# Optimization experiments

Hardware: AMD Instinct MI355X
Metric: run time of the kernel (lower is better)

## Reference

```python
import jax, jax.numpy as jnp
import numpy as np

D_MODEL = 512
N_HEADS = 8
D_K = D_MODEL // N_HEADS


def setup_inputs() -> dict:
    key = jax.random.key(0)
    ks = jax.random.split(key, 9)
    s = 1.0 / np.sqrt(D_MODEL)
    x = jax.random.normal(ks[0], (2, 4096, D_MODEL), dtype=jnp.float32)
    def lin(kw, kb):
        W = jax.random.uniform(kw, (D_MODEL, D_MODEL), jnp.float32, -s, s)
        b = jax.random.uniform(kb, (D_MODEL,), jnp.float32, -s, s)
        return W, b
    Wq, bq = lin(ks[1], ks[2])
    Wk, bk = lin(ks[3], ks[4])
    Wv, bv = lin(ks[5], ks[6])
    Wo, bo = lin(ks[7], ks[8])
    return {"x": x, "Wq": Wq, "bq": bq, "Wk": Wk, "bk": bk,
            "Wv": Wv, "bv": bv, "Wo": Wo, "bo": bo}


def reference(x, Wq, bq, Wk, bk, Wv, bv, Wo, bo):
    B, T, C = x.shape
    # project and split heads: [B, H, T, d_k]
    def heads(W, b):
        return (x @ W.T + b).reshape(B, T, N_HEADS, D_K).transpose(0, 2, 1, 3)
    q = heads(Wq, bq)
    k = heads(Wk, bk)
    v = heads(Wv, bv)
    scores = jnp.einsum('bhqd,bhkd->bhqk', q, k) / np.sqrt(D_K).astype(jnp.float32)
    attn = jax.nn.softmax(scores, axis=-1)  # dropout p=0 (eval)
    out = jnp.einsum('bhqk,bhkd->bhqd', attn, v)
    out = out.transpose(0, 2, 1, 3).reshape(B, T, C)
    return out @ Wo.T + bo
```

## Files before the change

kernel.cpp:

```cpp
#include <hip/hip_runtime.h>

typedef _Float16 f16x8 __attribute__((ext_vector_type(8)));
typedef _Float16 f16x4 __attribute__((ext_vector_type(4)));
typedef _Float16 f16x2 __attribute__((ext_vector_type(2)));
typedef __fp16 hf16x2 __attribute__((ext_vector_type(2)));
typedef float f32x4 __attribute__((ext_vector_type(4)));

__device__ __forceinline__ float fast_exp2(float x) {
#if __has_builtin(__builtin_amdgcn_exp2f)
  return __builtin_amdgcn_exp2f(x);
#else
  return exp2f(x);
#endif
}

__device__ __forceinline__ f16x2 pk_cvt(float a, float b) {
#if __has_builtin(__builtin_amdgcn_cvt_pkrtz)
  union { hf16x2 h; f16x2 f; } u;
  u.h = __builtin_amdgcn_cvt_pkrtz(a, b);
  return u.f;
#else
  f16x2 r; r[0] = (_Float16)a; r[1] = (_Float16)b; return r;
#endif
}

__global__ void cvt_all(const float* __restrict__ x,
                        const float* __restrict__ Wq, const float* __restrict__ Wk,
                        const float* __restrict__ Wv, const float* __restrict__ Wo,
                        _Float16* __restrict__ xf, _Float16* __restrict__ wf) {
  int g = blockIdx.x * blockDim.x + threadIdx.x;
  const float* src;
  _Float16* dst;
  if (g < 524288) {
    src = x + (size_t)g * 8;
    dst = xf + (size_t)g * 8;
  } else {
    int g2 = g - 524288;
    int z = g2 >> 15, off = g2 & 32767;
    const float* W = (z == 0) ? Wq : (z == 1) ? Wk : (z == 2) ? Wv : Wo;
    src = W + (size_t)off * 8;
    dst = wf + (size_t)z * 262144 + (size_t)off * 8;
  }
  f32x4 a = *(const f32x4*)src;
  f32x4 b = *(const f32x4*)(src + 4);
  f16x8 o;
  o[0] = (_Float16)a[0]; o[1] = (_Float16)a[1];
  o[2] = (_Float16)a[2]; o[3] = (_Float16)a[3];
  o[4] = (_Float16)b[0]; o[5] = (_Float16)b[1];
  o[6] = (_Float16)b[2]; o[7] = (_Float16)b[3];
  *(f16x8*)dst = o;
}

__global__ __launch_bounds__(256, 2)
void qkv_gemm(const _Float16* __restrict__ X, const _Float16* __restrict__ Wf,
              const float* __restrict__ bq, const float* __restrict__ bk,
              const float* __restrict__ bv, _Float16* __restrict__ dst3) {
  __shared__ __align__(16) _Float16 As[128][72];
  __shared__ __align__(16) _Float16 Bs[128][72];
  const int z = blockIdx.z;
  const _Float16* Wz = Wf + (size_t)z * 262144;
  const float* bias = (z == 0) ? bq : (z == 1 ? bk : bv);
  _Float16* dst = dst3 + (size_t)z * 4194304;
  const float scale = (z == 0) ? 0.18033688011112042f : 1.0f;

  const int t = threadIdx.x;
  const int lane = t & 63, wave = t >> 6;
  const int quad = lane >> 4, col = lane & 15;
  const int wm = (wave & 1) * 64, wn = (wave >> 1) * 64;
  const int m0 = blockIdx.x * 128, n0 = blockIdx.y * 128;

  f32x4 acc[4][4] = {};

  for (int k0 = 0; k0 < 512; k0 += 64) {
    __syncthreads();
#pragma unroll
    for (int i = 0; i < 4; i++) {
      int flat = i * 2048 + t * 8;
      int r = flat >> 6, c = flat & 63;
      *(f16x8*)&As[r][c] = *(const f16x8*)&X[(size_t)(m0 + r) * 512 + k0 + c];
      *(f16x8*)&Bs[r][c] = *(const f16x8*)&Wz[(size_t)(n0 + r) * 512 + k0 + c];
    }
    __syncthreads();
#pragma unroll
    for (int ks = 0; ks < 2; ks++) {
      f16x8 a[4], b[4];
#pragma unroll
      for (int i = 0; i < 4; i++) {
        a[i] = *(const f16x8*)&As[wm + i * 16 + col][ks * 32 + quad * 8];
        b[i] = *(const f16x8*)&Bs[wn + i * 16 + col][ks * 32 + quad * 8];
      }
#pragma unroll
      for (int mi = 0; mi < 4; mi++)
#pragma unroll
        for (int ni = 0; ni < 4; ni++)
          acc[mi][ni] = __builtin_amdgcn_mfma_f32_16x16x32_f16(a[mi], b[ni], acc[mi][ni], 0, 0, 0);
    }
  }

  if (z != 2) {
#pragma unroll
    for (int ni = 0; ni < 4; ni++) {
      int n = n0 + wn + ni * 16 + col;
      float bv_ = bias[n];
      int h = n >> 6, d = n & 63;
#pragma unroll
      for (int mi = 0; mi < 4; mi++) {
#pragma unroll
        for (int r = 0; r < 4; r++) {
          int m = m0 + wm + mi * 16 + quad * 4 + r;
          int b = m >> 12, tt = m & 4095;
          float v = (acc[mi][ni][r] + bv_) * scale;
          dst[((size_t)(b * 8 + h) * 4096 + tt) * 64 + d] = (_Float16)v;
        }
      }
    }
  } else {
#pragma unroll
    for (int ni = 0; ni < 4; ni++) {
      int n = n0 + wn + ni * 16 + col;
      float bv_ = bias[n];
      int h = n >> 6, d = n & 63;
#pragma unroll
      for (int mi = 0; mi < 4; mi++) {
        int m = m0 + wm + mi * 16 + quad * 4;
        int b = m >> 12, tt = m & 4095;
        f16x4 ov;
#pragma unroll
        for (int r = 0; r < 4; r++) ov[r] = (_Float16)(acc[mi][ni][r] + bv_);
        *(f16x4*)&dst[((size_t)((b * 8 + h) * 64 + d)) * 4096 + tt] = ov;
      }
    }
  }
}

__global__ __launch_bounds__(256, 2)
void attn_kernel(const _Float16* __restrict__ Q, const _Float16* __restrict__ K,
                 const _Float16* __restrict__ V, _Float16* __restrict__ O) {
  __shared__ __align__(16) _Float16 Ks[2][128][72];
  __shared__ __align__(16) _Float16 Vt[2][64][132];

  const int t = threadIdx.x;
  const int lane = t & 63, wave = t >> 6;
  const int quad = lane >> 4, col = lane & 15;
  const int bh = blockIdx.y;
  const int q0 = blockIdx.x * 128;
  const _Float16* Qb = Q + (size_t)bh * 4096 * 64;
  const _Float16* Kbh = K + (size_t)bh * 4096 * 64;
  const _Float16* Vg = V + (size_t)bh * 64 * 4096;

  const int sr = (t * 8) >> 6, sc = (t * 8) & 63;
  const int vrow = t >> 4, vcol = (t & 15) * 8;

  f16x8 qf[2][2];
#pragma unroll
  for (int mt = 0; mt < 2; mt++)
#pragma unroll
    for (int ks = 0; ks < 2; ks++)
      qf[mt][ks] = *(const f16x8*)&Qb[(size_t)(q0 + wave * 32 + mt * 16 + col) * 64 +
                                      ks * 32 + quad * 8];

  const f32x4 fz = {0.f, 0.f, 0.f, 0.f};

  f16x8 kreg[4], vreg[4];
#pragma unroll
  for (int i = 0; i < 4; i++)
    kreg[i] = *(const f16x8*)&Kbh[(size_t)(sr + 32 * i) * 64 + sc];
#pragma unroll
  for (int it = 0; it < 4; it++)
    vreg[it] = *(const f16x8*)&Vg[(size_t)(it * 16 + vrow) * 4096 + vcol];
#pragma unroll
  for (int i = 0; i < 4; i++)
    *(f16x8*)&Ks[0][sr + 32 * i][sc] = kreg[i];
#pragma unroll
  for (int it = 0; it < 4; it++) {
    f16x4 lo, hi;
#pragma unroll
    for (int u = 0; u < 4; u++) { lo[u] = vreg[it][u]; hi[u] = vreg[it][u + 4]; }
    *(f16x4*)&Vt[0][it * 16 + vrow][vcol] = lo;
    *(f16x4*)&Vt[0][it * 16 + vrow][vcol + 4] = hi;
  }
  __syncthreads();

  f32x4 o_acc[2][4] = {};
  float lsum[2] = {0.f, 0.f};

  for (int j = 0; j < 32; j++) {
    const int buf = j & 1;
    if (j + 1 < 32) {
      const _Float16* Kb = Kbh + (size_t)(j + 1) * 128 * 64;
#pragma unroll
      for (int i = 0; i < 4; i++)
        kreg[i] = *(const f16x8*)&Kb[(size_t)(sr + 32 * i) * 64 + sc];
#pragma unroll
      for (int it = 0; it < 4; it++)
        vreg[it] = *(const f16x8*)&Vg[(size_t)(it * 16 + vrow) * 4096 +
                                      (j + 1) * 128 + vcol];
    }

    f32x4 s[2][8];
    __builtin_amdgcn_s_setprio(1);
#pragma unroll
    for (int nt = 0; nt < 8; nt++) {
      f16x8 kf = *(const f16x8*)&Ks[buf][nt * 16 + col][quad * 8];
#pragma unroll
      for (int mt = 0; mt < 2; mt++)
        s[mt][nt] = __builtin_amdgcn_mfma_f32_16x16x32_f16(kf, qf[mt][0], fz, 0, 0, 0);
    }
#pragma unroll
    for (int nt = 0; nt < 8; nt++) {
      f16x8 kf = *(const f16x8*)&Ks[buf][nt * 16 + col][32 + quad * 8];
#pragma unroll
      for (int mt = 0; mt < 2; mt++)
        s[mt][nt] = __builtin_amdgcn_mfma_f32_16x16x32_f16(kf, qf[mt][1], s[mt][nt], 0, 0, 0);
    }
    __builtin_amdgcn_s_setprio(0);

    f16x4 pf[2][8];
#pragma unroll
    for (int mt = 0; mt < 2; mt++) {
#pragma unroll
      for (int nt = 0; nt < 8; nt++) {
        float p0 = fast_exp2(s[mt][nt][0]);
        float p1 = fast_exp2(s[mt][nt][1]);
        float p2 = fast_exp2(s[mt][nt][2]);
        float p3 = fast_exp2(s[mt][nt][3]);
        lsum[mt] += (p0 + p1) + (p2 + p3);
        union { f16x4 v4; f16x2 v2[2]; } u;
        u.v2[0] = pk_cvt(p0, p1);
        u.v2[1] = pk_cvt(p2, p3);
        pf[mt][nt] = u.v4;
      }
    }

    __builtin_amdgcn_s_setprio(1);
#pragma unroll
    for (int nt = 0; nt < 8; nt++) {
#pragma unroll
      for (int dt = 0; dt < 4; dt++) {
        f16x4 vf = *(const f16x4*)&Vt[buf][dt * 16 + col][nt * 16 + quad * 4];
#pragma unroll
        for (int mt = 0; mt < 2; mt++)
          o_acc[mt][dt] = __builtin_amdgcn_mfma_f32_16x16x16f16(vf, pf[mt][nt], o_acc[mt][dt], 0, 0, 0);
      }
    }
    __builtin_amdgcn_s_setprio(0);

    if (j + 1 < 32) {
      const int nb = buf ^ 1;
#pragma unroll
      for (int i = 0; i < 4; i++)
        *(f16x8*)&Ks[nb][sr + 32 * i][sc] = kreg[i];
#pragma unroll
      for (int it = 0; it < 4; it++) {
        f16x4 lo, hi;
#pragma unroll
        for (int u = 0; u < 4; u++) { lo[u] = vreg[it][u]; hi[u] = vreg[it][u + 4]; }
        *(f16x4*)&Vt[nb][it * 16 + vrow][vcol] = lo;
        *(f16x4*)&Vt[nb][it * 16 + vrow][vcol + 4] = hi;
      }
      __syncthreads();
    }
  }

  const int b = bh >> 3, h = bh & 7;
#pragma unroll
  for (int mt = 0; mt < 2; mt++) {
    float l = lsum[mt];
    l += __shfl_xor(l, 16, 64);
    l += __shfl_xor(l, 32, 64);
    int row = q0 + wave * 32 + mt * 16 + col;
    float inv = 1.0f / l;
#pragma unroll
    for (int dt = 0; dt < 4; dt++) {
      f16x4 ov;
#pragma unroll
      for (int r = 0; r < 4; r++) ov[r] = (_Float16)(o_acc[mt][dt][r] * inv);
      *(f16x4*)&O[((size_t)(b * 4096 + row)) * 512 + h * 64 + dt * 16 + quad * 4] = ov;
    }
  }
}

__global__ __launch_bounds__(256, 2)
void out_gemm(const _Float16* __restrict__ X, const _Float16* __restrict__ Wo,
              const float* __restrict__ bias, float* __restrict__ out) {
  __shared__ __align__(16) _Float16 As[128][72];
  __shared__ __align__(16) _Float16 Bs[128][72];
  const int t = threadIdx.x;
  const int lane = t & 63, wave = t >> 6;
  const int quad = lane >> 4, col = lane & 15;
  const int wm = (wave & 1) * 64, wn = (wave >> 1) * 64;
  const int m0 = blockIdx.x * 128, n0 = blockIdx.y * 128;

  f32x4 acc[4][4] = {};

  for (int k0 = 0; k0 < 512; k0 += 64) {
    __syncthreads();
#pragma unroll
    for (int i = 0; i < 4; i++) {
      int flat = i * 2048 + t * 8;
      int r = flat >> 6, c = flat & 63;
      *(f16x8*)&As[r][c] = *(const f16x8*)&X[(size_t)(m0 + r) * 512 + k0 + c];
      *(f16x8*)&Bs[r][c] = *(const f16x8*)&Wo[(size_t)(n0 + r) * 512 + k0 + c];
    }
    __syncthreads();
#pragma unroll
    for (int ks = 0; ks < 2; ks++) {
      f16x8 a[4], b[4];
#pragma unroll
      for (int i = 0; i < 4; i++) {
        a[i] = *(const f16x8*)&As[wm + i * 16 + col][ks * 32 + quad * 8];
        b[i] = *(const f16x8*)&Bs[wn + i * 16 + col][ks * 32 + quad * 8];
      }
#pragma unroll
      for (int mi = 0; mi < 4; mi++)
#pragma unroll
        for (int ni = 0; ni < 4; ni++)
          acc[mi][ni] = __builtin_amdgcn_mfma_f32_16x16x32_f16(a[mi], b[ni], acc[mi][ni], 0, 0, 0);
    }
  }

#pragma unroll
  for (int ni = 0; ni < 4; ni++) {
    int n = n0 + wn + ni * 16 + col;
    float bv_ = bias[n];
#pragma unroll
    for (int mi = 0; mi < 4; mi++) {
#pragma unroll
      for (int r = 0; r < 4; r++) {
        int m = m0 + wm + mi * 16 + quad * 4 + r;
        out[(size_t)m * 512 + n] = acc[mi][ni][r] + bv_;
      }
    }
  }
}

extern "C" void kernel_launch(void* const* d_in, const int* in_sizes, int n_in,
                              void* d_out, int out_size, void* d_ws, size_t ws_size,
                              hipStream_t stream) {
  const float* x  = (const float*)d_in[0];
  const float* Wq = (const float*)d_in[1];
  const float* bq = (const float*)d_in[2];
  const float* Wk = (const float*)d_in[3];
  const float* bk = (const float*)d_in[4];
  const float* Wv = (const float*)d_in[5];
  const float* bv = (const float*)d_in[6];
  const float* Wo = (const float*)d_in[7];
  const float* bo = (const float*)d_in[8];

  char* ws = (char*)d_ws;
  _Float16* xf  = (_Float16*)(ws);
  _Float16* wf  = (_Float16*)(ws + (8u << 20));
  _Float16* qkv = (_Float16*)(ws + (10u << 20));
  _Float16* ao  = (_Float16*)(ws);

  cvt_all<<<2560, 256, 0, stream>>>(x, Wq, Wk, Wv, Wo, xf, wf);

  qkv_gemm<<<dim3(64, 4, 3), 256, 0, stream>>>(xf, wf, bq, bk, bv, qkv);

  attn_kernel<<<dim3(32, 16), 256, 0, stream>>>(qkv, qkv + 4194304,
                                                qkv + 2 * 4194304, ao);

  out_gemm<<<dim3(64, 4), 256, 0, stream>>>(ao, wf + 3 * 262144, bo,
                                            (float*)d_out);
}
```

Baseline: 202.0 us.

## Shrink attention tiles to 64 queries and 64 keys for higher occupancy

The attention kernel now handles 64 query rows per block (16 per wave) and streams K/V in 64-key tiles instead of 128. Register use and shared memory per block drop, launch bounds rise to 4 blocks per SIMD-group, and the grid doubles to 1024 blocks to better fill the GPU. In exchange, each K/V tile is reused by half as many queries, which doubles global and LDS traffic per query, and the loop runs twice as many iterations with a barrier in each.

```diff
diff --git a/kernel.cpp b/kernel.cpp
--- a/kernel.cpp
+++ b/kernel.cpp
@@ -133,150 +133,136 @@
   }
 }
 
-__global__ __launch_bounds__(256, 2)
+__global__ __launch_bounds__(256, 4)
 void attn_kernel(const _Float16* __restrict__ Q, const _Float16* __restrict__ K,
                  const _Float16* __restrict__ V, _Float16* __restrict__ O) {
-  __shared__ __align__(16) _Float16 Ks[2][128][72];
-  __shared__ __align__(16) _Float16 Vt[2][64][132];
+  __shared__ __align__(16) _Float16 Ks[2][64][72];
+  __shared__ __align__(16) _Float16 Vt[2][64][68];
 
   const int t = threadIdx.x;
   const int lane = t & 63, wave = t >> 6;
   const int quad = lane >> 4, col = lane & 15;
   const int bh = blockIdx.y;
-  const int q0 = blockIdx.x * 128;
+  const int q0 = blockIdx.x * 64;
   const _Float16* Qb = Q + (size_t)bh * 4096 * 64;
   const _Float16* Kbh = K + (size_t)bh * 4096 * 64;
   const _Float16* Vg = V + (size_t)bh * 64 * 4096;
 
-  const int sr = (t * 8) >> 6, sc = (t * 8) & 63;
-  const int vrow = t >> 4, vcol = (t & 15) * 8;
-
-  f16x8 qf[2][2];
-#pragma unroll
-  for (int mt = 0; mt < 2; mt++)
-#pragma unroll
-    for (int ks = 0; ks < 2; ks++)
-      qf[mt][ks] = *(const f16x8*)&Qb[(size_t)(q0 + wave * 32 + mt * 16 + col) * 64 +
-                                      ks * 32 + quad * 8];
+  const int sr = t >> 3, sc = (t & 7) * 8;
+  const int vrow = t >> 3, vcol = (t & 7) * 8;
+
+  f16x8 qf[2];
+#pragma unroll
+  for (int ks = 0; ks < 2; ks++)
+    qf[ks] = *(const f16x8*)&Qb[(size_t)(q0 + wave * 16 + col) * 64 +
+                                ks * 32 + quad * 8];
 
   const f32x4 fz = {0.f, 0.f, 0.f, 0.f};
 
-  f16x8 kreg[4], vreg[4];
-#pragma unroll
-  for (int i = 0; i < 4; i++)
+  f16x8 kreg[2], vreg[2];
+#pragma unroll
+  for (int i = 0; i < 2; i++)
     kreg[i] = *(const f16x8*)&Kbh[(size_t)(sr + 32 * i) * 64 + sc];
 #pragma unroll
-  for (int it = 0; it < 4; it++)
-    vreg[it] = *(const f16x8*)&Vg[(size_t)(it * 16 + vrow) * 4096 + vcol];
-#pragma unroll
-  for (int i = 0; i < 4; i++)
+  for (int it = 0; it < 2; it++)
+    vreg[it] = *(const f16x8*)&Vg[(size_t)(it * 32 + vrow) * 4096 + vcol];
+#pragma unroll
+  for (int i = 0; i < 2; i++)
     *(f16x8*)&Ks[0][sr + 32 * i][sc] = kreg[i];
 #pragma unroll
-  for (int it = 0; it < 4; it++) {
+  for (int it = 0; it < 2; it++) {
     f16x4 lo, hi;
 #pragma unroll
     for (int u = 0; u < 4; u++) { lo[u] = vreg[it][u]; hi[u] = vreg[it][u + 4]; }
-    *(f16x4*)&Vt[0][it * 16 + vrow][vcol] = lo;
-    *(f16x4*)&Vt[0][it * 16 + vrow][vcol + 4] = hi;
+    *(f16x4*)&Vt[0][it * 32 + vrow][vcol] = lo;
+    *(f16x4*)&Vt[0][it * 32 + vrow][vcol + 4] = hi;
   }
   __syncthreads();
 
-  f32x4 o_acc[2][4] = {};
-  float lsum[2] = {0.f, 0.f};
-
-  for (int j = 0; j < 32; j++) {
+  f32x4 o_acc[4] = {};
+  float lsum = 0.f;
+
+  for (int j = 0; j < 64; j++) {
     const int buf = j & 1;
-    if (j + 1 < 32) {
-      const _Float16* Kb = Kbh + (size_t)(j + 1) * 128 * 64;
-#pragma unroll
-      for (int i = 0; i < 4; i++)
+    if (j + 1 < 64) {
+      const _Float16* Kb = Kbh + (size_t)(j + 1) * 64 * 64;
+#pragma unroll
+      for (int i = 0; i < 2; i++)
         kreg[i] = *(const f16x8*)&Kb[(size_t)(sr + 32 * i) * 64 + sc];
 #pragma unroll
-      for (int it = 0; it < 4; it++)
-        vreg[it] = *(const f16x8*)&Vg[(size_t)(it * 16 + vrow) * 4096 +
-                                      (j + 1) * 128 + vcol];
-    }
-
-    f32x4 s[2][8];
+      for (int it = 0; it < 2; it++)
+        vreg[it] = *(const f16x8*)&Vg[(size_t)(it * 32 + vrow) * 4096 +
+                                      (j + 1) * 64 + vcol];
+    }
+
+    f32x4 s[4];
     __builtin_amdgcn_s_setprio(1);
 #pragma unroll
-    for (int nt = 0; nt < 8; nt++) {
+    for (int nt = 0; nt < 4; nt++) {
       f16x8 kf = *(const f16x8*)&Ks[buf][nt * 16 + col][quad * 8];
-#pragma unroll
-      for (int mt = 0; mt < 2; mt++)
-        s[mt][nt] = __builtin_amdgcn_mfma_f32_16x16x32_f16(kf, qf[mt][0], fz, 0, 0, 0);
-    }
-#pragma unroll
-    for (int nt = 0; nt < 8; nt++) {
+      s[nt] = __builtin_amdgcn_mfma_f32_16x16x32_f16(kf, qf[0], fz, 0, 0, 0);
+    }
+#pragma unroll
+    for (int nt = 0; nt < 4; nt++) {
       f16x8 kf = *(const f16x8*)&Ks[buf][nt * 16 + col][32 + quad * 8];
-#pragma unroll
-      for (int mt = 0; mt < 2; mt++)
-        s[mt][nt] = __builtin_amdgcn_mfma_f32_16x16x32_f16(kf, qf[mt][1], s[mt][nt], 0, 0, 0);
+      s[nt] = __builtin_amdgcn_mfma_f32_16x16x32_f16(kf, qf[1], s[nt], 0, 0, 0);
     }
     __builtin_amdgcn_s_setprio(0);
 
-    f16x4 pf[2][8];
-#pragma unroll
-    for (int mt = 0; mt < 2; mt++) {
-#pragma unroll
-      for (int nt = 0; nt < 8; nt++) {
-        float p0 = fast_exp2(s[mt][nt][0]);
-        float p1 = fast_exp2(s[mt][nt][1]);
-        float p2 = fast_exp2(s[mt][nt][2]);
-        float p3 = fast_exp2(s[mt][nt][3]);
-        lsum[mt] += (p0 + p1) + (p2 + p3);
-        union { f16x4 v4; f16x2 v2[2]; } u;
-        u.v2[0] = pk_cvt(p0, p1);
-        u.v2[1] = pk_cvt(p2, p3);
-        pf[mt][nt] = u.v4;
-      }
+    f16x4 pf[4];
+#pragma unroll
+    for (int nt = 0; nt < 4; nt++) {
+      float p0 = fast_exp2(s[nt][0]);
+      float p1 = fast_exp2(s[nt][1]);
+      float p2 = fast_exp2(s[nt][2]);
+      float p3 = fast_exp2(s[nt][3]);
+      lsum += (p0 + p1) + (p2 + p3);
+      union { f16x4 v4; f16x2 v2[2]; } u;
+      u.v2[0] = pk_cvt(p0, p1);
+      u.v2[1] = pk_cvt(p2, p3);
+      pf[nt] = u.v4;
     }
 
     __builtin_amdgcn_s_setprio(1);
 #pragma unroll
-    for (int nt = 0; nt < 8; nt++) {
+    for (int nt = 0; nt < 4; nt++) {
 #pragma unroll
       for (int dt = 0; dt < 4; dt++) {
         f16x4 vf = *(const f16x4*)&Vt[buf][dt * 16 + col][nt * 16 + quad * 4];
-#pragma unroll
-        for (int mt = 0; mt < 2; mt++)
-          o_acc[mt][dt] = __builtin_amdgcn_mfma_f32_16x16x16f16(vf, pf[mt][nt], o_acc[mt][dt], 0, 0, 0);
+        o_acc[dt] = __builtin_amdgcn_mfma_f32_16x16x16f16(vf, pf[nt], o_acc[dt], 0, 0, 0);
       }
     }
     __builtin_amdgcn_s_setprio(0);
 
-    if (j + 1 < 32) {
+    if (j + 1 < 64) {
       const int nb = buf ^ 1;
 #pragma unroll
-      for (int i = 0; i < 4; i++)
+      for (int i = 0; i < 2; i++)
         *(f16x8*)&Ks[nb][sr + 32 * i][sc] = kreg[i];
 #pragma unroll
-      for (int it = 0; it < 4; it++) {
+      for (int it = 0; it < 2; it++) {
         f16x4 lo, hi;
 #pragma unroll
         for (int u = 0; u < 4; u++) { lo[u] = vreg[it][u]; hi[u] = vreg[it][u + 4]; }
-        *(f16x4*)&Vt[nb][it * 16 + vrow][vcol] = lo;
-        *(f16x4*)&Vt[nb][it * 16 + vrow][vcol + 4] = hi;
+        *(f16x4*)&Vt[nb][it * 32 + vrow][vcol] = lo;
+        *(f16x4*)&Vt[nb][it * 32 + vrow][vcol + 4] = hi;
       }
       __syncthreads();
     }
   }
 
   const int b = bh >> 3, h = bh & 7;
-#pragma unroll
-  for (int mt = 0; mt < 2; mt++) {
-    float l = lsum[mt];
-    l += __shfl_xor(l, 16, 64);
-    l += __shfl_xor(l, 32, 64);
-    int row = q0 + wave * 32 + mt * 16 + col;
-    float inv = 1.0f / l;
-#pragma unroll
-    for (int dt = 0; dt < 4; dt++) {
-      f16x4 ov;
-#pragma unroll
-      for (int r = 0; r < 4; r++) ov[r] = (_Float16)(o_acc[mt][dt][r] * inv);
-      *(f16x4*)&O[((size_t)(b * 4096 + row)) * 512 + h * 64 + dt * 16 + quad * 4] = ov;
-    }
+  float l = lsum;
+  l += __shfl_xor(l, 16, 64);
+  l += __shfl_xor(l, 32, 64);
+  const int row = q0 + wave * 16 + col;
+  const float inv = 1.0f / l;
+#pragma unroll
+  for (int dt = 0; dt < 4; dt++) {
+    f16x4 ov;
+#pragma unroll
+    for (int r = 0; r < 4; r++) ov[r] = (_Float16)(o_acc[dt][r] * inv);
+    *(f16x4*)&O[((size_t)(b * 4096 + row)) * 512 + h * 64 + dt * 16 + quad * 4] = ov;
   }
 }
 
@@ -357,7 +343,7 @@
 
   qkv_gemm<<<dim3(64, 4, 3), 256, 0, stream>>>(xf, wf, bq, bk, bv, qkv);
 
-  attn_kernel<<<dim3(32, 16), 256, 0, stream>>>(qkv, qkv + 4194304,
+  attn_kernel<<<dim3(64, 16), 256, 0, stream>>>(qkv, qkv + 4194304,
                                                 qkv + 2 * 4194304, ao);
 
   out_gemm<<<dim3(64, 4), 256, 0, stream>>>(ao, wf + 3 * 262144, bo,
```

New measurement: 225.4 us. +11.6%, slower.

## Use 16x16x32 MFMA for PV with permlane32 swap and swizzled V tile

Applied to the files above, without the earlier changes.

The P·V product in the attention kernel now uses the K=32 f16 MFMA instead of pairs of K=16 MFMAs. The P fragments from two adjacent score tiles are recombined across half-waves with v_permlane32_swap. The V tile in shared memory is stored with a column swizzle so that each lane can read 8 contiguous halves matching the new operand layout. This is meant to halve the MFMA instruction count and the LDS read count for PV. In exchange it adds permlane swaps and a padded, swizzled V layout whose index mapping must be exactly right.

```diff
diff --git a/kernel.cpp b/kernel.cpp
--- a/kernel.cpp
+++ b/kernel.cpp
@@ -22,6 +22,14 @@
 #else
   f16x2 r; r[0] = (_Float16)a; r[1] = (_Float16)b; return r;
 #endif
+}
+
+__device__ __forceinline__ void qswap32(int& x, int& y) {
+  asm("v_permlane32_swap_b32 %0, %1" : "+v"(x), "+v"(y));
+}
+
+__device__ __forceinline__ int swz23(int c) {
+  return (c & ~12) | ((c & 4) << 1) | ((c & 8) >> 1);
 }
 
 __global__ void cvt_all(const float* __restrict__ x,
@@ -137,7 +145,7 @@
 void attn_kernel(const _Float16* __restrict__ Q, const _Float16* __restrict__ K,
                  const _Float16* __restrict__ V, _Float16* __restrict__ O) {
   __shared__ __align__(16) _Float16 Ks[2][128][72];
-  __shared__ __align__(16) _Float16 Vt[2][64][132];
+  __shared__ __align__(16) _Float16 Vt[2][64][136];
 
   const int t = threadIdx.x;
   const int lane = t & 63, wave = t >> 6;
@@ -150,6 +158,8 @@
 
   const int sr = (t * 8) >> 6, sc = (t * 8) & 63;
   const int vrow = t >> 4, vcol = (t & 15) * 8;
+  const int vc0 = swz23(vcol);
+  const int vc1 = swz23(vcol + 4);
 
   f16x8 qf[2][2];
 #pragma unroll
@@ -176,8 +186,8 @@
     f16x4 lo, hi;
 #pragma unroll
     for (int u = 0; u < 4; u++) { lo[u] = vreg[it][u]; hi[u] = vreg[it][u + 4]; }
-    *(f16x4*)&Vt[0][it * 16 + vrow][vcol] = lo;
-    *(f16x4*)&Vt[0][it * 16 + vrow][vcol + 4] = hi;
+    *(f16x4*)&Vt[0][it * 16 + vrow][vc0] = lo;
+    *(f16x4*)&Vt[0][it * 16 + vrow][vc1] = hi;
   }
   __syncthreads();
 
@@ -234,13 +244,25 @@
 
     __builtin_amdgcn_s_setprio(1);
 #pragma unroll
-    for (int nt = 0; nt < 8; nt++) {
+    for (int u = 0; u < 4; u++) {
+      f16x8 p8[2];
+#pragma unroll
+      for (int mt = 0; mt < 2; mt++) {
+        union { f16x4 v; int d[2]; } X, Y;
+        X.v = pf[mt][2 * u]; Y.v = pf[mt][2 * u + 1];
+        int x0 = X.d[0], y0 = Y.d[0], x1 = X.d[1], y1 = Y.d[1];
+        qswap32(x0, y0);
+        qswap32(x1, y1);
+        union { int d[4]; f16x8 v; } P;
+        P.d[0] = x0; P.d[1] = x1; P.d[2] = y0; P.d[3] = y1;
+        p8[mt] = P.v;
+      }
 #pragma unroll
       for (int dt = 0; dt < 4; dt++) {
-        f16x4 vf = *(const f16x4*)&Vt[buf][dt * 16 + col][nt * 16 + quad * 4];
+        f16x8 vf = *(const f16x8*)&Vt[buf][dt * 16 + col][u * 32 + quad * 8];
 #pragma unroll
         for (int mt = 0; mt < 2; mt++)
-          o_acc[mt][dt] = __builtin_amdgcn_mfma_f32_16x16x16f16(vf, pf[mt][nt], o_acc[mt][dt], 0, 0, 0);
+          o_acc[mt][dt] = __builtin_amdgcn_mfma_f32_16x16x32_f16(vf, p8[mt], o_acc[mt][dt], 0, 0, 0);
       }
     }
     __builtin_amdgcn_s_setprio(0);
@@ -255,8 +277,8 @@
         f16x4 lo, hi;
 #pragma unroll
         for (int u = 0; u < 4; u++) { lo[u] = vreg[it][u]; hi[u] = vreg[it][u + 4]; }
-        *(f16x4*)&Vt[nb][it * 16 + vrow][vcol] = lo;
-        *(f16x4*)&Vt[nb][it * 16 + vrow][vcol + 4] = hi;
+        *(f16x4*)&Vt[nb][it * 16 + vrow][vc0] = lo;
+        *(f16x4*)&Vt[nb][it * 16 + vrow][vc1] = hi;
       }
       __syncthreads();
     }
```

New measurement: 199.0 us. No clear change (-1.5%).
